# Optimization experiments

Hardware: AMD Instinct MI355X
Metric: run time of the kernel (lower is better)

The kernel has to match this reference:

```python
import jax, jax.numpy as jnp
import numpy as np

WIN = 11
SIGMA = 1.5
K1, K2 = 0.01, 0.03
DATA_RANGE = 1.0


def _gauss1d(size, sigma):
    coords = jnp.arange(size, dtype=jnp.float32) - size // 2
    g = jnp.exp(-(coords ** 2) / (2.0 * sigma ** 2))
    return g / g.sum()


def _blur(x, g):
    # Separable depthwise Gaussian blur, VALID padding, matching F.conv2d(groups=C).
    C = x.shape[1]
    w = g.astype(x.dtype)
    kh = jnp.broadcast_to(w.reshape(1, 1, WIN, 1), (C, 1, WIN, 1))  # blur along H
    kw = jnp.broadcast_to(w.reshape(1, 1, 1, WIN), (C, 1, 1, WIN))  # blur along W
    dn = ('NCHW', 'OIHW', 'NCHW')
    out = jax.lax.conv_general_dilated(x, kh, (1, 1), 'VALID',
                                       dimension_numbers=dn, feature_group_count=C)
    out = jax.lax.conv_general_dilated(out, kw, (1, 1), 'VALID',
                                       dimension_numbers=dn, feature_group_count=C)
    return out


def setup_inputs() -> dict:
    key = jax.random.key(0)
    k1, k2 = jax.random.split(key)
    shape = (16, 3, 512, 512)
    image1 = jax.random.uniform(k1, shape, dtype=jnp.float32)
    image2 = jax.random.uniform(k2, shape, dtype=jnp.float32)
    window = _gauss1d(WIN, SIGMA)
    return {"image1": image1, "image2": image2, "window": window}


def reference(image1, image2, window):
    c1 = (K1 * DATA_RANGE) ** 2
    c2 = (K2 * DATA_RANGE) ** 2
    mu1 = _blur(image1, window)
    mu2 = _blur(image2, window)
    mu1_sq = mu1 * mu1
    mu2_sq = mu2 * mu2
    mu1_mu2 = mu1 * mu2
    sigma1_sq = _blur(image1 * image1, window) - mu1_sq
    sigma2_sq = _blur(image2 * image2, window) - mu2_sq
    sigma12 = _blur(image1 * image2, window) - mu1_mu2
    cs_map = (2.0 * sigma12 + c2) / (sigma1_sq + sigma2_sq + c2)
    ssim_map = (2.0 * mu1_mu2 + c1) / (mu1_sq + mu2_sq + c1) * cs_map
    # flatten(2).mean(-1) then .mean() over (B,C) == full mean (uniform sizes)
    return ssim_map.mean()
```

## Files before the change

kernel.cpp:

```cpp
#include <hip/hip_runtime.h>

#define WIN   11
#define IW    512
#define IH    512
#define OW    502
#define OH    502
#define NCH   48
#define TW    118
#define SWC   128
#define SWP   134
#define CH    8
#define NCHUNK 4
#define SLABH (CH*NCHUNK)
#define NGX   5
#define NGY   16

typedef float v2f __attribute__((ext_vector_type(2)));

__device__ __forceinline__ float fast_rcp(float x) {
    return __builtin_amdgcn_rcpf(x);
}

__device__ __forceinline__ v2f pk_fma(v2f a, v2f b, v2f c) {
    v2f d;
    asm("v_pk_fma_f32 %0, %1, %2, %3" : "=v"(d) : "v"(a), "v"(b), "v"(c));
    return d;
}

template<bool EDGE>
__device__ __forceinline__ void ssim_slab(const float* __restrict__ p1,
                                          const float* __restrict__ p2,
                                          const v2f (&wv)[WIN],
                                          v2f (*vbuf)[CH][SWP],
                                          int x0, int y0, int tid, float& acc)
{
    const int c = tid;
    int gx = x0 + c;
    if (EDGE) gx = min(gx, IW - 1);

    v2f h[10];
#pragma unroll
    for (int j = 0; j < 10; ++j) {
        int gy = y0 + j; if (EDGE) gy = min(gy, IH - 1);
        const int gidx = gy * IW + gx;
        h[j].x = p1[gidx];
        h[j].y = p2[gidx];
    }

    const int rh = tid & 7;
    const int g  = tid >> 3;
    const int xs = g * 8;
    const float c1 = 0.0001f;
    const float c2 = 0.0009f;

#pragma unroll
    for (int ci = 0; ci < NCHUNK; ++ci) {
        const int jbase = y0 + 10 + ci * CH;
        v2f n[CH];
#pragma unroll
        for (int j = 0; j < CH; ++j) {
            int gy = jbase + j; if (EDGE) gy = min(gy, IH - 1);
            const int gidx = gy * IW + gx;
            n[j].x = p1[gidx];
            n[j].y = p2[gidx];
        }

        v2f accA[CH], accB[CH];
#pragma unroll
        for (int r = 0; r < CH; ++r) {
            accA[r] = (v2f){0.f, 0.f};
            accB[r] = (v2f){0.f, 0.f};
        }
#pragma unroll
        for (int j = 0; j < CH + 10; ++j) {
            v2f ab = (j < 10) ? h[j] : n[j - 10];
            v2f st;
            st.x = fmaf(ab.x, ab.x, ab.y * ab.y);
            st.y = ab.x * ab.y;
#pragma unroll
            for (int k = 0; k < WIN; ++k) {
                const int r = j - k;
                if (r >= 0 && r < CH) {
                    accA[r] = pk_fma(wv[k], ab, accA[r]);
                    accB[r] = pk_fma(wv[k], st, accB[r]);
                }
            }
            if (j >= 10) {
                vbuf[0][j - 10][c] = accA[j - 10];
                vbuf[1][j - 10][c] = accB[j - 10];
            }
        }
#pragma unroll
        for (int j = 0; j < 10; ++j)
            h[j] = (j < 2) ? h[8 + j] : n[j - 2];

        __syncthreads();

        if (g < 15) {
            v2f resA[8], resB[8];
#pragma unroll
            for (int q = 0; q < 2; ++q) {
                v2f x2[18];
                const v2f* src = &vbuf[q][rh][xs];
#pragma unroll
                for (int t = 0; t < 18; ++t)
                    x2[t] = src[t];
#pragma unroll
                for (int o = 0; o < 8; ++o) {
                    v2f s = {0.f, 0.f};
#pragma unroll
                    for (int k = 0; k < WIN; ++k)
                        s = pk_fma(wv[k], x2[o + k], s);
                    if (q == 0) resA[o] = s; else resB[o] = s;
                }
            }

            const int oy = y0 + ci * CH + rh;
#pragma unroll
            for (int o = 0; o < 8; ++o) {
                const int tc = xs + o;
                bool valid = (tc < TW);
                if (EDGE) valid = valid && (oy < OH) && ((x0 + tc) < OW);
                if (valid) {
                    float m1 = resA[o].x, m2 = resA[o].y;
                    float mu11 = m1 * m1, mu22 = m2 * m2, mu12 = m1 * m2;
                    float sAB = resB[o].x - mu11 - mu22;
                    float s12 = resB[o].y - mu12;
                    float num = (2.f * mu12 + c1) * (2.f * s12 + c2);
                    float den = (mu11 + mu22 + c1) * (sAB + c2);
                    acc += num * fast_rcp(den);
                }
            }
        }
        __syncthreads();
    }
}

__global__ __launch_bounds__(128, 2)
void ssim_fused_kernel(const float* __restrict__ img1,
                       const float* __restrict__ img2,
                       const float* __restrict__ win,
                       float* __restrict__ partial)
{
    __shared__ __align__(16) v2f vbuf[2][CH][SWP];
    __shared__ float wavesum[2];

    const int tid = threadIdx.x;
    const int ch = blockIdx.z;
    const int x0 = blockIdx.x * TW;
    const int y0 = blockIdx.y * SLABH;
    const float* __restrict__ p1 = img1 + (size_t)ch * (IW * IH);
    const float* __restrict__ p2 = img2 + (size_t)ch * (IW * IH);

    v2f wv[WIN];
#pragma unroll
    for (int k = 0; k < WIN; ++k) {
        float wk = win[k];
        wv[k].x = wk; wv[k].y = wk;
    }

    float acc = 0.f;
    const bool edge = (blockIdx.x == gridDim.x - 1) || (blockIdx.y == gridDim.y - 1);
    if (edge) ssim_slab<true >(p1, p2, wv, vbuf, x0, y0, tid, acc);
    else      ssim_slab<false>(p1, p2, wv, vbuf, x0, y0, tid, acc);

#pragma unroll
    for (int off = 32; off > 0; off >>= 1)
        acc += __shfl_down(acc, off, 64);
    if ((tid & 63) == 0) wavesum[tid >> 6] = acc;
    __syncthreads();
    if (tid == 0) {
        partial[(size_t)blockIdx.z * (gridDim.x * gridDim.y)
                + blockIdx.y * gridDim.x + blockIdx.x] = wavesum[0] + wavesum[1];
    }
}

__global__ __launch_bounds__(256)
void reduce_partials_kernel(const float* __restrict__ partial, int n4,
                            float* __restrict__ out, double inv_count)
{
    __shared__ double sd[256];
    const float4* p4 = reinterpret_cast<const float4*>(partial);
    double s = 0.0;
    for (int i = threadIdx.x; i < n4; i += 256) {
        float4 f = p4[i];
        s += (double)f.x + (double)f.y + (double)f.z + (double)f.w;
    }
    sd[threadIdx.x] = s;
    __syncthreads();
    for (int off = 128; off > 0; off >>= 1) {
        if (threadIdx.x < off) sd[threadIdx.x] += sd[threadIdx.x + off];
        __syncthreads();
    }
    if (threadIdx.x == 0)
        out[0] = (float)(sd[0] * inv_count);
}

extern "C" void kernel_launch(void* const* d_in, const int* in_sizes, int n_in,
                              void* d_out, int out_size, void* d_ws, size_t ws_size,
                              hipStream_t stream)
{
    const float* img1 = (const float*)d_in[0];
    const float* img2 = (const float*)d_in[1];
    const float* win  = (const float*)d_in[2];
    float* out = (float*)d_out;
    float* partial = (float*)d_ws;

    dim3 grid(NGX, NGY, NCH);
    dim3 block(128);

    ssim_fused_kernel<<<grid, block, 0, stream>>>(img1, img2, win, partial);

    const int nblocks = NGX * NGY * NCH;
    const double inv_count = 1.0 / ((double)NCH * OW * OH);
    reduce_partials_kernel<<<1, 256, 0, stream>>>(partial, nblocks / 4, out, inv_count);
}
```

Measured before the change: 51.31 us.

## Double-buffer row loads across chunks and double slab height per block

Rows for the next chunk are now loaded into registers before the current chunk's vertical and horizontal blur runs, using two ping-pong register arrays so global load latency overlaps compute. Each block also covers twice as many rows (8 chunks instead of 4), halving the grid height and the redundant 10-row halo reads. This costs more live VGPRs, which may cause spills under the 2-waves launch bound, and cuts the block count, which lowers parallelism.

```diff
diff --git a/kernel.cpp b/kernel.cpp
--- a/kernel.cpp
+++ b/kernel.cpp
@@ -10,10 +10,10 @@
 #define SWC   128
 #define SWP   134
 #define CH    8
-#define NCHUNK 4
+#define NCHUNK 8
 #define SLABH (CH*NCHUNK)
 #define NGX   5
-#define NGY   16
+#define NGY   8
 
 typedef float v2f __attribute__((ext_vector_type(2)));
 
@@ -25,6 +25,104 @@
     v2f d;
     asm("v_pk_fma_f32 %0, %1, %2, %3" : "=v"(d) : "v"(a), "v"(b), "v"(c));
     return d;
+}
+
+template<bool EDGE>
+__device__ __forceinline__ void load_rows(const float* __restrict__ p1,
+                                          const float* __restrict__ p2,
+                                          int gx, int jbase, v2f (&dst)[CH])
+{
+#pragma unroll
+    for (int j = 0; j < CH; ++j) {
+        int gy = jbase + j; if (EDGE) gy = min(gy, IH - 1);
+        const int gidx = gy * IW + gx;
+        dst[j].x = p1[gidx];
+        dst[j].y = p2[gidx];
+    }
+}
+
+template<bool EDGE>
+__device__ __forceinline__ void chunk_step(const float* __restrict__ p1,
+                                           const float* __restrict__ p2,
+                                           bool pf, int gx, int jbase_next,
+                                           v2f (&h)[10], v2f (&cur)[CH], v2f (&nxt)[CH],
+                                           const v2f (&wv)[WIN],
+                                           v2f (*vbuf)[CH][SWP],
+                                           int c, int rh, int g, int xs,
+                                           int oy0, int x0, float& acc)
+{
+    if (pf) load_rows<EDGE>(p1, p2, gx, jbase_next, nxt);
+
+    v2f accA[CH], accB[CH];
+#pragma unroll
+    for (int r = 0; r < CH; ++r) {
+        accA[r] = (v2f){0.f, 0.f};
+        accB[r] = (v2f){0.f, 0.f};
+    }
+#pragma unroll
+    for (int j = 0; j < CH + 10; ++j) {
+        v2f ab = (j < 10) ? h[j] : cur[j - 10];
+        v2f st;
+        st.x = fmaf(ab.x, ab.x, ab.y * ab.y);
+        st.y = ab.x * ab.y;
+#pragma unroll
+        for (int k = 0; k < WIN; ++k) {
+            const int r = j - k;
+            if (r >= 0 && r < CH) {
+                accA[r] = pk_fma(wv[k], ab, accA[r]);
+                accB[r] = pk_fma(wv[k], st, accB[r]);
+            }
+        }
+        if (j >= 10) {
+            vbuf[0][j - 10][c] = accA[j - 10];
+            vbuf[1][j - 10][c] = accB[j - 10];
+        }
+    }
+#pragma unroll
+    for (int j = 0; j < 10; ++j)
+        h[j] = (j < 2) ? h[8 + j] : cur[j - 2];
+
+    __syncthreads();
+
+    if (g < 15) {
+        const float c1 = 0.0001f;
+        const float c2 = 0.0009f;
+        v2f resA[8], resB[8];
+#pragma unroll
+        for (int q = 0; q < 2; ++q) {
+            v2f x2[18];
+            const v2f* src = &vbuf[q][rh][xs];
+#pragma unroll
+            for (int t = 0; t < 18; ++t)
+                x2[t] = src[t];
+#pragma unroll
+            for (int o = 0; o < 8; ++o) {
+                v2f s = {0.f, 0.f};
+#pragma unroll
+                for (int k = 0; k < WIN; ++k)
+                    s = pk_fma(wv[k], x2[o + k], s);
+                if (q == 0) resA[o] = s; else resB[o] = s;
+            }
+        }
+
+        const int oy = oy0 + rh;
+#pragma unroll
+        for (int o = 0; o < 8; ++o) {
+            const int tc = xs + o;
+            bool valid = (tc < TW);
+            if (EDGE) valid = valid && (oy < OH) && ((x0 + tc) < OW);
+            if (valid) {
+                float m1 = resA[o].x, m2 = resA[o].y;
+                float mu11 = m1 * m1, mu22 = m2 * m2, mu12 = m1 * m2;
+                float sAB = resB[o].x - mu11 - mu22;
+                float s12 = resB[o].y - mu12;
+                float num = (2.f * mu12 + c1) * (2.f * s12 + c2);
+                float den = (mu11 + mu22 + c1) * (sAB + c2);
+                acc += num * fast_rcp(den);
+            }
+        }
+    }
+    __syncthreads();
 }
 
 template<bool EDGE>
@@ -46,93 +144,22 @@
         h[j].x = p1[gidx];
         h[j].y = p2[gidx];
     }
+    v2f nA[CH], nB[CH];
+    load_rows<EDGE>(p1, p2, gx, y0 + 10, nA);
 
     const int rh = tid & 7;
     const int g  = tid >> 3;
     const int xs = g * 8;
-    const float c1 = 0.0001f;
-    const float c2 = 0.0009f;
-
-#pragma unroll
-    for (int ci = 0; ci < NCHUNK; ++ci) {
-        const int jbase = y0 + 10 + ci * CH;
-        v2f n[CH];
-#pragma unroll
-        for (int j = 0; j < CH; ++j) {
-            int gy = jbase + j; if (EDGE) gy = min(gy, IH - 1);
-            const int gidx = gy * IW + gx;
-            n[j].x = p1[gidx];
-            n[j].y = p2[gidx];
-        }
-
-        v2f accA[CH], accB[CH];
-#pragma unroll
-        for (int r = 0; r < CH; ++r) {
-            accA[r] = (v2f){0.f, 0.f};
-            accB[r] = (v2f){0.f, 0.f};
-        }
-#pragma unroll
-        for (int j = 0; j < CH + 10; ++j) {
-            v2f ab = (j < 10) ? h[j] : n[j - 10];
-            v2f st;
-            st.x = fmaf(ab.x, ab.x, ab.y * ab.y);
-            st.y = ab.x * ab.y;
-#pragma unroll
-            for (int k = 0; k < WIN; ++k) {
-                const int r = j - k;
-                if (r >= 0 && r < CH) {
-                    accA[r] = pk_fma(wv[k], ab, accA[r]);
-                    accB[r] = pk_fma(wv[k], st, accB[r]);
-                }
-            }
-            if (j >= 10) {
-                vbuf[0][j - 10][c] = accA[j - 10];
-                vbuf[1][j - 10][c] = accB[j - 10];
-            }
-        }
-#pragma unroll
-        for (int j = 0; j < 10; ++j)
-            h[j] = (j < 2) ? h[8 + j] : n[j - 2];
-
-        __syncthreads();
-
-        if (g < 15) {
-            v2f resA[8], resB[8];
-#pragma unroll
-            for (int q = 0; q < 2; ++q) {
-                v2f x2[18];
-                const v2f* src = &vbuf[q][rh][xs];
-#pragma unroll
-                for (int t = 0; t < 18; ++t)
-                    x2[t] = src[t];
-#pragma unroll
-                for (int o = 0; o < 8; ++o) {
-                    v2f s = {0.f, 0.f};
-#pragma unroll
-                    for (int k = 0; k < WIN; ++k)
-                        s = pk_fma(wv[k], x2[o + k], s);
-                    if (q == 0) resA[o] = s; else resB[o] = s;
-                }
-            }
-
-            const int oy = y0 + ci * CH + rh;
-#pragma unroll
-            for (int o = 0; o < 8; ++o) {
-                const int tc = xs + o;
-                bool valid = (tc < TW);
-                if (EDGE) valid = valid && (oy < OH) && ((x0 + tc) < OW);
-                if (valid) {
-                    float m1 = resA[o].x, m2 = resA[o].y;
-                    float mu11 = m1 * m1, mu22 = m2 * m2, mu12 = m1 * m2;
-                    float sAB = resB[o].x - mu11 - mu22;
-                    float s12 = resB[o].y - mu12;
-                    float num = (2.f * mu12 + c1) * (2.f * s12 + c2);
-                    float den = (mu11 + mu22 + c1) * (sAB + c2);
-                    acc += num * fast_rcp(den);
-                }
-            }
-        }
-        __syncthreads();
+
+#pragma unroll
+    for (int cp = 0; cp < NCHUNK / 2; ++cp) {
+        const int ci0 = 2 * cp, ci1 = 2 * cp + 1;
+        chunk_step<EDGE>(p1, p2, true, gx, y0 + 10 + (ci0 + 1) * CH,
+                         h, nA, nB, wv, vbuf, c, rh, g, xs,
+                         y0 + ci0 * CH, x0, acc);
+        chunk_step<EDGE>(p1, p2, (ci1 + 1 < NCHUNK), gx, y0 + 10 + (ci1 + 1) * CH,
+                         h, nB, nA, wv, vbuf, c, rh, g, xs,
+                         y0 + ci1 * CH, x0, acc);
     }
 }
 
```

After: 58.77 us. +14.5%, slower.
